# Performance work log

Hardware: AMD Instinct MI355X
Metric: run time of the kernel (lower is better)

## Reference

```python
import jax, jax.numpy as jnp
import numpy as np

NBITS = 4
OUT_F = 2048
IN_F = 2048


def _bit_ste(w, nbits):
    # clamp to [-1,1], quantize magnitude to nbits levels, keep sign
    step = float(2 ** nbits - 1)
    w = jnp.clip(w, -1.0, 1.0)
    return jnp.round(jnp.abs(w) * step) / step * jnp.sign(w)


def setup_inputs() -> dict:
    key = jax.random.key(0)
    ks = jax.random.split(key, 6)
    ex = np.arange(NBITS - 1, -1, -1)
    exps = jnp.asarray(2.0 ** ex / (2.0 ** NBITS - 1), dtype=jnp.float32)
    inp = {
        "input": jax.random.normal(ks[0], (8, 2048, IN_F), dtype=jnp.float32),
        # bit-plane weights: sigmoid of these gives soft bits in (0,1)
        "pweight": jax.random.normal(ks[1], (OUT_F, IN_F, NBITS), dtype=jnp.float32),
        "nweight": jax.random.normal(ks[2], (OUT_F, IN_F, NBITS), dtype=jnp.float32),
        "exps": exps,
        "bexps": exps,
        "mask_weight": jnp.ones((NBITS,), dtype=jnp.float32),  # init.constant_(1)
        "scale": jnp.array([0.05], dtype=jnp.float32),
        "pbias": jax.random.uniform(ks[3], (OUT_F, NBITS), dtype=jnp.float32, minval=0.0, maxval=float(2 ** NBITS - 1)) // 1.0 % 2.0,
        "nbias": jax.random.uniform(ks[4], (OUT_F, NBITS), dtype=jnp.float32, minval=0.0, maxval=float(2 ** NBITS - 1)) // 1.0 % 2.0,
        "biasscale": jnp.array([0.05], dtype=jnp.float32),
    }
    return inp


def reference(input, pweight, nweight, exps, bexps, mask_weight, scale, pbias, nbias, biasscale):
    temp = 1.0
    # temp_s and mask_discrete are all-ones buffers -> identity factors
    mask = jax.nn.sigmoid(mask_weight)                      # [N]
    soft = jax.nn.sigmoid(temp * pweight) - jax.nn.sigmoid(temp * nweight)  # [O,I,N]
    weight = jnp.einsum('oin,n->oi', soft, exps * mask) * scale[0]          # [O,I]
    bias_raw = jnp.einsum('on,n->o', pbias - nbias, bexps)  # [O]
    bias = _bit_ste(bias_raw, NBITS) * biasscale[0]
    # F.linear: y = x @ W^T + b
    return jnp.einsum('bsi,oi->bso', input, weight) + bias
```

## Files before the change

### kernel.cpp

```cpp
#include <hip/hip_runtime.h>
#include <hip/hip_bf16.h>
#include <stdint.h>

#define M_DIM 16384
#define N_DIM 2048
#define K_DIM 2048

typedef __attribute__((ext_vector_type(8))) __bf16 bf16x8;
typedef __attribute__((ext_vector_type(4))) float f32x4;

__device__ __forceinline__ unsigned short f2bf(float f) {
  unsigned int u = __builtin_bit_cast(unsigned int, f);
  u += 0x7FFFu + ((u >> 16) & 1u);
  return (unsigned short)(u >> 16);
}

__device__ __forceinline__ float sigmoidf_(float x) {
  return 1.0f / (1.0f + __expf(-x));
}

__global__ __launch_bounds__(256) void convert_x(const float4* __restrict__ x,
                                                 uint4* __restrict__ xb) {
  int idx = blockIdx.x * 256 + threadIdx.x;
  float4 a = x[idx * 2];
  float4 b = x[idx * 2 + 1];
  uint4 r;
  r.x = (unsigned)f2bf(a.x) | ((unsigned)f2bf(a.y) << 16);
  r.y = (unsigned)f2bf(a.z) | ((unsigned)f2bf(a.w) << 16);
  r.z = (unsigned)f2bf(b.x) | ((unsigned)f2bf(b.y) << 16);
  r.w = (unsigned)f2bf(b.z) | ((unsigned)f2bf(b.w) << 16);
  xb[idx] = r;
}

__global__ __launch_bounds__(256) void make_w(const float4* __restrict__ pw,
                                              const float4* __restrict__ nw,
                                              const float* __restrict__ exps,
                                              const float* __restrict__ maskw,
                                              const float* __restrict__ scale,
                                              unsigned short* __restrict__ wout) {
  const int beta = blockIdx.x;
  const int xcd = beta & 7;
  const int j = beta >> 3;
  const int o = xcd * 256 + (j >> 3);
  const int iblk = j & 7;
  int idx = (o * 2048 + iblk * 256) + threadIdx.x;
  float4 p = pw[idx];
  float4 n = nw[idx];
  float s = scale[0];
  float c0 = sigmoidf_(maskw[0]) * exps[0] * s;
  float c1 = sigmoidf_(maskw[1]) * exps[1] * s;
  float c2 = sigmoidf_(maskw[2]) * exps[2] * s;
  float c3 = sigmoidf_(maskw[3]) * exps[3] * s;
  float w = (sigmoidf_(p.x) - sigmoidf_(n.x)) * c0
          + (sigmoidf_(p.y) - sigmoidf_(n.y)) * c1
          + (sigmoidf_(p.z) - sigmoidf_(n.z)) * c2
          + (sigmoidf_(p.w) - sigmoidf_(n.w)) * c3;
  wout[idx] = f2bf(w);
}

__global__ __launch_bounds__(256) void make_bias(const float* __restrict__ pb,
                                                 const float* __restrict__ nb,
                                                 const float* __restrict__ bexps,
                                                 const float* __restrict__ bscale,
                                                 float* __restrict__ bias) {
  int o = blockIdx.x * 256 + threadIdx.x;
  if (o < N_DIM) {
    float x = 0.f;
#pragma unroll
    for (int n = 0; n < 4; ++n) x += (pb[o * 4 + n] - nb[o * 4 + n]) * bexps[n];
    float xc = fminf(fmaxf(x, -1.f), 1.f);
    float mag = rintf(fabsf(xc) * 15.f) * (1.f / 15.f);
    float sgn = (xc > 0.f) ? 1.f : ((xc < 0.f) ? -1.f : 0.f);
    bias[o] = mag * sgn * bscale[0];
  }
}


#define BM 256
#define BN 256
#define BK 32
#define NT (K_DIM / BK)
#define NBUF 4

__device__ __forceinline__ void gload16(const void* g, void* l) {
  __builtin_amdgcn_global_load_lds(
      (const __attribute__((address_space(1))) unsigned int*)g,
      (__attribute__((address_space(3))) unsigned int*)l, 16, 0, 0);
}

#define VMCNT(n) asm volatile("s_waitcnt vmcnt(" #n ")" ::: "memory")
#define BAR() __builtin_amdgcn_s_barrier()

__global__ __launch_bounds__(512, 2) void gemm_bias(const unsigned short* __restrict__ X,
                                                    const unsigned short* __restrict__ W,
                                                    const float* __restrict__ bias,
                                                    float* __restrict__ out) {
  __shared__ unsigned short sA[NBUF][128 * 64];
  __shared__ unsigned short sB[NBUF][128 * 64];

  const int tid = threadIdx.x;
  const int bn = (int)blockIdx.x & 7;
  const int bm = (int)blockIdx.x >> 3;
  const int row0 = bm * BM, col0 = bn * BN;

  const int w = tid >> 6, l = tid & 63;
  const int wr = w >> 2;
  const int wc = w & 3;
  const int lr = l & 15;
  const int lk4 = l >> 4;
  const int lr7 = lr & 7;

  const unsigned short* Ag = X + (size_t)row0 * K_DIM;
  const unsigned short* Bg = W + (size_t)col0 * K_DIM;

  const int s_frl = tid >> 3;
  const int s_pre = (tid & 7) ^ ((tid >> 3) & 7);
  const int s_rglo = 128 * (s_pre >> 2);
  const int s_k = (s_pre & 3) * 8;
  const int s_dst = tid * 8;

  auto stage = [&](unsigned short* lbase, const unsigned short* gbase,
                   int rr, int tk) {
    gload16(gbase + (size_t)(rr + s_frl + s_rglo) * K_DIM + tk * BK + s_k,
            lbase + rr * 64 + s_dst);
  };

  auto rdA = [&](const unsigned short* base, int mf) -> bf16x8 {
    int fr = mf * 16 + lr;
    int slot = (lk4 + 4 * wr) ^ lr7;
    return *(const bf16x8*)&base[fr * 64 + slot * 8];
  };
  auto rdB = [&](const unsigned short* base, int nf) -> bf16x8 {
    int fr = (wc & 1) * 64 + nf * 16 + lr;
    int slot = (lk4 + 4 * (wc >> 1)) ^ lr7;
    return *(const bf16x8*)&base[fr * 64 + slot * 8];
  };

  f32x4 acc[8][4] = {};
  bf16x8 a[8], b[4];

#pragma unroll
  for (int pt = 0; pt < 3; ++pt) {
    stage(sA[pt], Ag, 0, pt);
    stage(sA[pt], Ag, 64, pt);
    stage(sB[pt], Bg, 0, pt);
    stage(sB[pt], Bg, 64, pt);
  }
  VMCNT(8);
  BAR();

  for (int t = 0; t < NT; ++t) {
    const unsigned short* pa = sA[t & 3];
    const unsigned short* pb = sB[t & 3];
    unsigned short* qa = sA[(t + 3) & 3];
    unsigned short* qb = sB[(t + 3) & 3];
    const int tk3 = (t + 3) & (NT - 1);
#pragma unroll
    for (int mf = 0; mf < 8; ++mf) a[mf] = rdA(pa, mf);
#pragma unroll
    for (int nf = 0; nf < 4; ++nf) b[nf] = rdB(pb, nf);

    stage(qa, Ag, 0, tk3);
    stage(qa, Ag, 64, tk3);
    stage(qb, Bg, 0, tk3);
    stage(qb, Bg, 64, tk3);

    __builtin_amdgcn_s_setprio(1);
#pragma unroll
    for (int mf = 0; mf < 8; ++mf)
#pragma unroll
      for (int nf = 0; nf < 4; ++nf)
        acc[mf][nf] = __builtin_amdgcn_mfma_f32_16x16x32_bf16(
            a[mf], b[nf], acc[mf][nf], 0, 0, 0);
    __builtin_amdgcn_s_setprio(0);

    VMCNT(8);
    BAR();
  }

  float bv[4];
#pragma unroll
  for (int nf = 0; nf < 4; ++nf) bv[nf] = bias[col0 + wc * 64 + nf * 16 + lr];
  const int orow = lk4 * 4;
#pragma unroll
  for (int mf = 0; mf < 8; ++mf) {
#pragma unroll
    for (int nf = 0; nf < 4; ++nf) {
      const int colg = col0 + wc * 64 + nf * 16 + lr;
#pragma unroll
      for (int r = 0; r < 4; ++r) {
        int rowg = row0 + wr * 128 + mf * 16 + orow + r;
        out[(size_t)rowg * N_DIM + colg] = acc[mf][nf][r] + bv[nf];
      }
    }
  }
}

extern "C" void kernel_launch(void* const* d_in, const int* in_sizes, int n_in,
                              void* d_out, int out_size, void* d_ws, size_t ws_size,
                              hipStream_t stream) {
  const float* input  = (const float*)d_in[0];
  const float* pweight = (const float*)d_in[1];
  const float* nweight = (const float*)d_in[2];
  const float* exps   = (const float*)d_in[3];
  const float* bexps  = (const float*)d_in[4];
  const float* maskw  = (const float*)d_in[5];
  const float* scale  = (const float*)d_in[6];
  const float* pbias  = (const float*)d_in[7];
  const float* nbias  = (const float*)d_in[8];
  const float* bscale = (const float*)d_in[9];
  float* out = (float*)d_out;

  unsigned short* Xb = (unsigned short*)d_ws;
  unsigned short* Wb = (unsigned short*)((char*)d_ws + (size_t)M_DIM * K_DIM * 2);
  float* bias = (float*)((char*)d_ws + (size_t)M_DIM * K_DIM * 2 + (size_t)N_DIM * K_DIM * 2);

  convert_x<<<(M_DIM * (size_t)K_DIM) / 8 / 256, 256, 0, stream>>>((const float4*)input, (uint4*)Xb);
  make_w<<<((size_t)N_DIM * K_DIM) / 256, 256, 0, stream>>>(
      (const float4*)pweight, (const float4*)nweight, exps, maskw, scale, Wb);
  make_bias<<<(N_DIM + 255) / 256, 256, 0, stream>>>(pbias, nbias, bexps, bscale, bias);

  dim3 grid((M_DIM / BM) * (N_DIM / BN));
  gemm_bias<<<grid, 512, 0, stream>>>(Xb, Wb, bias, out);
}
```

Baseline: 201.7 us.

## Split GEMM waves into two roles that stagger LDS reads and MFMA

Waves are divided into two roles by a checkerboard of wave indices. Role-0 waves read the current tile's fragments and then run MFMAs. Role-1 waves run MFMAs on fragments they preloaded, then read the next tile's fragments before the barrier. The goal is to spread LDS traffic and matrix-core work over time so that not every wave hits LDS at once. Making this safe requires a tighter vmcnt wait (4 instead of 8), which shortens how far ahead global prefetches can run, and role-1 waves hold an extra fragment set in registers.

```diff
diff --git a/kernel.cpp b/kernel.cpp
--- a/kernel.cpp
+++ b/kernel.cpp
@@ -109,6 +109,7 @@
   const int lr = l & 15;
   const int lk4 = l >> 4;
   const int lr7 = lr & 7;
+  const int role = (w & 1) ^ ((w >> 2) & 1);
 
   const unsigned short* Ag = X + (size_t)row0 * K_DIM;
   const unsigned short* Bg = W + (size_t)col0 * K_DIM;
@@ -139,6 +140,14 @@
   f32x4 acc[8][4] = {};
   bf16x8 a[8], b[4];
 
+#define DO_MFMA()                                                             \
+  __builtin_amdgcn_s_setprio(1);                                              \
+  _Pragma("unroll") for (int mf = 0; mf < 8; ++mf)                            \
+  _Pragma("unroll") for (int nf = 0; nf < 4; ++nf)                            \
+      acc[mf][nf] = __builtin_amdgcn_mfma_f32_16x16x32_bf16(                  \
+          a[mf], b[nf], acc[mf][nf], 0, 0, 0);                                \
+  __builtin_amdgcn_s_setprio(0);
+
 #pragma unroll
   for (int pt = 0; pt < 3; ++pt) {
     stage(sA[pt], Ag, 0, pt);
@@ -146,37 +155,51 @@
     stage(sB[pt], Bg, 0, pt);
     stage(sB[pt], Bg, 64, pt);
   }
-  VMCNT(8);
+  VMCNT(4);
   BAR();
+
+  if (role) {
+#pragma unroll
+    for (int mf = 0; mf < 8; ++mf) a[mf] = rdA(sA[0], mf);
+#pragma unroll
+    for (int nf = 0; nf < 4; ++nf) b[nf] = rdB(sB[0], nf);
+  }
 
   for (int t = 0; t < NT; ++t) {
     const unsigned short* pa = sA[t & 3];
     const unsigned short* pb = sB[t & 3];
+    const unsigned short* na = sA[(t + 1) & 3];
+    const unsigned short* nb = sB[(t + 1) & 3];
     unsigned short* qa = sA[(t + 3) & 3];
     unsigned short* qb = sB[(t + 3) & 3];
     const int tk3 = (t + 3) & (NT - 1);
-#pragma unroll
-    for (int mf = 0; mf < 8; ++mf) a[mf] = rdA(pa, mf);
-#pragma unroll
-    for (int nf = 0; nf < 4; ++nf) b[nf] = rdB(pb, nf);
-
-    stage(qa, Ag, 0, tk3);
-    stage(qa, Ag, 64, tk3);
-    stage(qb, Bg, 0, tk3);
-    stage(qb, Bg, 64, tk3);
-
-    __builtin_amdgcn_s_setprio(1);
-#pragma unroll
-    for (int mf = 0; mf < 8; ++mf)
-#pragma unroll
-      for (int nf = 0; nf < 4; ++nf)
-        acc[mf][nf] = __builtin_amdgcn_mfma_f32_16x16x32_bf16(
-            a[mf], b[nf], acc[mf][nf], 0, 0, 0);
-    __builtin_amdgcn_s_setprio(0);
-
-    VMCNT(8);
+
+    if (role == 0) {
+#pragma unroll
+      for (int mf = 0; mf < 8; ++mf) a[mf] = rdA(pa, mf);
+#pragma unroll
+      for (int nf = 0; nf < 4; ++nf) b[nf] = rdB(pb, nf);
+      stage(qa, Ag, 0, tk3);
+      stage(qa, Ag, 64, tk3);
+      stage(qb, Bg, 0, tk3);
+      stage(qb, Bg, 64, tk3);
+      DO_MFMA();
+    } else {
+      DO_MFMA();
+      stage(qa, Ag, 0, tk3);
+      stage(qa, Ag, 64, tk3);
+      stage(qb, Bg, 0, tk3);
+      stage(qb, Bg, 64, tk3);
+#pragma unroll
+      for (int mf = 0; mf < 8; ++mf) a[mf] = rdA(na, mf);
+#pragma unroll
+      for (int nf = 0; nf < 4; ++nf) b[nf] = rdB(nb, nf);
+    }
+
+    VMCNT(4);
     BAR();
   }
+  VMCNT(0);
 
   float bv[4];
 #pragma unroll
@@ -194,6 +217,7 @@
       }
     }
   }
+#undef DO_MFMA
 }
 
 extern "C" void kernel_launch(void* const* d_in, const int* in_sizes, int n_in,
```

Result: slower. 222.6 us (+10.4%).
